# Performance work log

Measured on AMD Instinct MI355X. Metric: run time of the kernel, lower is better.

## Reference

```python
import jax, jax.numpy as jnp
import numpy as np

NQ = 14            # qubits = ceil(log2(16384))
DIM = 2 ** NQ
OUT = 1000         # out_features (slice last OUT probs)


def _apply_ry(state, theta, axis):
    """Apply RY(theta) on the qubit at `axis` of state shaped (B, 2,...,2).
    RY = [[cos(t/2), -sin(t/2)], [sin(t/2), cos(t/2)]] (real)."""
    c = jnp.cos(theta / 2)
    s = jnp.sin(theta / 2)
    x = jnp.moveaxis(state, axis, -1)
    x0, x1 = x[..., 0], x[..., 1]
    y = jnp.stack([c * x0 - s * x1, s * x0 + c * x1], axis=-1)
    return jnp.moveaxis(y, -1, axis)


def _apply_cz(state, axis):
    """CZ on adjacent qubits (axis, axis+1): flip sign of |11> amplitudes."""
    sign = jnp.ones((2, 2), state.dtype).at[1, 1].set(-1.0)
    shape = [1] * state.ndim
    shape[axis] = 2
    shape[axis + 1] = 2
    return state * sign.reshape(shape)


def _circuit(inp, weights, bias):
    B, F = inp.shape
    # AmplitudeEmbedding(pad_with=1, normalize=True)
    if F < DIM:
        inp = jnp.pad(inp, ((0, 0), (0, DIM - F)), constant_values=1.0)
    norm = jnp.sqrt(jnp.sum(inp * inp, axis=1, keepdims=True))
    state = (inp / norm).reshape((B,) + (2,) * NQ)
    # SimplifiedTwoDesign: initial RY layer (bias)
    for w in range(NQ):
        state = _apply_ry(state, bias[w], 1 + w)
    # entangling layers: even CZ/RY block then odd CZ/RY block
    nlayer = weights.shape[0]
    for l in range(nlayer):
        for start in (0, 1):
            for i in range(start, NQ - 1, 2):
                state = _apply_cz(state, 1 + i)
                state = _apply_ry(state, weights[l, i, 0], 1 + i)
                state = _apply_ry(state, weights[l, i, 1], 1 + i + 1)
    amps = state.reshape(B, DIM)
    probs = amps * amps  # real statevector -> |amp|^2
    return probs[:, -OUT:]


def setup_inputs() -> dict:
    key = jax.random.key(0)
    k1, k2, k3 = jax.random.split(key, 3)
    return {
        "input": jax.random.normal(k1, (512, 16384), dtype=jnp.float32),
        "weights": jax.random.normal(k2, (2, NQ - 1, 2), dtype=jnp.float32),
        "bias": jax.random.normal(k3, (NQ,), dtype=jnp.float32),
    }


def reference(input, weights, bias):
    return _circuit(input, weights, bias)
```

## Files before the change

kernel.cpp:

```cpp
#include <hip/hip_runtime.h>

#define NQ 14
#define DIM 16384
#define OUT_N 1000

using v2f = __attribute__((ext_vector_type(2))) float;

__host__ __device__ constexpr int WI(int l, int i, int k) {
    return 14 + (l * 13 + i) * 2 + k;
}

__device__ __forceinline__ int swzM(int e) { return e ^ ((e >> 6) & 31); }
__device__ __forceinline__ int swzB(int a) { return a ^ ((a >> 5) & 31); }

template<int B, int NP>
__device__ __forceinline__ void ry(v2f* x, float c, float s) {
    if constexpr (B == 0) {
#pragma unroll
        for (int p = 0; p < NP; ++p) {
            float a0 = x[p].x, a1 = x[p].y;
            x[p].x = c * a0 - s * a1;
            x[p].y = s * a0 + c * a1;
        }
    } else {
        constexpr int pb = B - 1;
#pragma unroll
        for (int m = 0; m < NP / 2; ++m) {
            int p0 = ((m >> pb) << (pb + 1)) | (m & ((1 << pb) - 1));
            int p1 = p0 | (1 << pb);
            v2f lo = x[p0], hi = x[p1];
            x[p0] = lo * c - hi * s;
            x[p1] = hi * c + lo * s;
        }
    }
}

template<int BH, int BL, int NP>
__device__ __forceinline__ void cz(v2f* x) {
    static_assert(BH > BL, "");
    if constexpr (BL >= 1) {
#pragma unroll
        for (int p = 0; p < NP; ++p)
            if (((p >> (BH - 1)) & 1) && ((p >> (BL - 1)) & 1)) x[p] = -x[p];
    } else {
#pragma unroll
        for (int p = 0; p < NP; ++p)
            if ((p >> (BH - 1)) & 1) x[p].y = -x[p].y;
    }
}

#define BLK(BH, I0, I1, NP)                                       \
    cz<BH, BH - 1, NP>(x);                                        \
    { float2 cc = csl[I0]; ry<BH, NP>(x, cc.x, cc.y); }           \
    { float2 cd = csl[I1]; ry<BH - 1, NP>(x, cd.x, cd.y); }

__global__ __launch_bounds__(256, 2)
void qnn_fused(const float* __restrict__ in, const float* __restrict__ wts,
               const float* __restrict__ bias, float* __restrict__ out) {
    __shared__ float lds[DIM];
    __shared__ float2 csl[66];
    __shared__ float red[4];

    const int t = threadIdx.x;
    const int b = blockIdx.x;

    if (t < 66) {
        float th = (t < NQ) ? bias[t] : wts[t - NQ];
        csl[t] = make_float2(cosf(0.5f * th), sinf(0.5f * th));
    }

    v2f x[32];
    { const float4* __restrict__ src4 = (const float4*)(in + (size_t)b * DIM + t * 64);
#pragma unroll
      for (int i = 0; i < 16; ++i) {
          float4 f = src4[i];
          x[2 * i].x = f.x;     x[2 * i].y = f.y;
          x[2 * i + 1].x = f.z; x[2 * i + 1].y = f.w;
      } }

    float pp = 0.f;
#pragma unroll
    for (int p = 0; p < 32; ++p) pp = fmaf(x[p].x, x[p].x, fmaf(x[p].y, x[p].y, pp));
#pragma unroll
    for (int d = 32; d; d >>= 1) pp += __shfl_xor(pp, d);
    if ((t & 63) == 0) red[t >> 6] = pp;
    __syncthreads();
    const float scale = 1.0f / sqrtf(red[0] + red[1] + red[2] + red[3]);

    { float2 cc;
      cc = csl[8];  ry<5, 32>(x, cc.x, cc.y);
      cc = csl[9];  ry<4, 32>(x, cc.x, cc.y);
      cc = csl[10]; ry<3, 32>(x, cc.x, cc.y);
      cc = csl[11]; ry<2, 32>(x, cc.x, cc.y);
      cc = csl[12]; ry<1, 32>(x, cc.x, cc.y);
      cc = csl[13]; ry<0, 32>(x, cc.x, cc.y); }
    BLK(5, WI(0,8,0),  WI(0,8,1),  32)
    BLK(3, WI(0,10,0), WI(0,10,1), 32)
    BLK(1, WI(0,12,0), WI(0,12,1), 32)
    BLK(4, WI(0,9,0),  WI(0,9,1),  32)
    BLK(2, WI(0,11,0), WI(0,11,1), 32)
    BLK(3, WI(1,10,0), WI(1,10,1), 32)
    BLK(1, WI(1,12,0), WI(1,12,1), 32)
    BLK(2, WI(1,11,0), WI(1,11,1), 32)

#pragma unroll
    for (int r = 0; r < 64; ++r)
        lds[swzM((t << 6) | r)] = (r & 1) ? x[r >> 1].y : x[r >> 1].x;
    __syncthreads();
#pragma unroll
    for (int r = 0; r < 64; ++r) {
        float v = lds[swzM((r << 8) | t)];
        if (r & 1) x[r >> 1].y = v; else x[r >> 1].x = v;
    }

    { float2 cc;
      cc = csl[0]; ry<5, 32>(x, cc.x, cc.y);
      cc = csl[1]; ry<4, 32>(x, cc.x, cc.y);
      cc = csl[2]; ry<3, 32>(x, cc.x, cc.y);
      cc = csl[3]; ry<2, 32>(x, cc.x, cc.y);
      cc = csl[4]; ry<1, 32>(x, cc.x, cc.y);
      cc = csl[5]; ry<0, 32>(x, cc.x, cc.y); }
    BLK(5, WI(0,0,0), WI(0,0,1), 32)
    BLK(3, WI(0,2,0), WI(0,2,1), 32)
    BLK(1, WI(0,4,0), WI(0,4,1), 32)
    BLK(4, WI(0,1,0), WI(0,1,1), 32)
    BLK(2, WI(0,3,0), WI(0,3,1), 32)
    BLK(5, WI(1,0,0), WI(1,0,1), 32)
    BLK(3, WI(1,2,0), WI(1,2,1), 32)
    BLK(4, WI(1,1,0), WI(1,1,1), 32)

    __syncthreads();
#pragma unroll
    for (int p = 28; p < 32; ++p) {
        lds[swzB(((2 * p - 56) << 8) | t)] = x[p].x * scale;
        lds[swzB(((2 * p - 55) << 8) | t)] = x[p].y * scale;
    }
    __syncthreads();

    if (t < 64) {
        const int s = t;
#pragma unroll
        for (int l = 0; l < 32; ++l) {
            float v = lds[swzB((l << 6) | s)];
            if (l & 1) x[l >> 1].y = v; else x[l >> 1].x = v;
        }
        { float2 cc;
          cc = csl[6]; ry<1, 16>(x, cc.x, cc.y);
          cc = csl[7]; ry<0, 16>(x, cc.x, cc.y); }
        BLK(1, WI(0,6,0), WI(0,6,1), 16)
        BLK(2, WI(0,5,0), WI(0,5,1), 16)
        BLK(3, WI(1,4,0), WI(1,4,1), 16)
        BLK(4, WI(1,3,0), WI(1,3,1), 16)
#pragma unroll
        for (int l = 0; l < 32; ++l)
            lds[swzB((l << 6) | s)] = (l & 1) ? x[l >> 1].y : x[l >> 1].x;
    }
    __syncthreads();
    if (t < 64) {
        const int s = t;
#pragma unroll
        for (int l = 0; l < 32; ++l) {
            float v = lds[swzB(((s >> 4) << 9) | (l << 4) | (s & 15))];
            if (l & 1) x[l >> 1].y = v; else x[l >> 1].x = v;
        }
        BLK(2, WI(0,7,0), WI(0,7,1), 16)
        BLK(3, WI(1,6,0), WI(1,6,1), 16)
        BLK(1, WI(1,8,0), WI(1,8,1), 16)
        BLK(4, WI(1,5,0), WI(1,5,1), 16)
        BLK(2, WI(1,7,0), WI(1,7,1), 16)
#pragma unroll
        for (int l = 0; l < 32; ++l)
            lds[swzB(((s >> 4) << 9) | (l << 4) | (s & 15))] =
                (l & 1) ? x[l >> 1].y : x[l >> 1].x;
    }
    __syncthreads();
    if (t < 64) {
        const int s = t;
#pragma unroll
        for (int l = 0; l < 32; ++l) {
            float v = lds[swzB(((s >> 2) << 7) | (l << 2) | (s & 3))];
            if (l & 1) x[l >> 1].y = v; else x[l >> 1].x = v;
        }
        BLK(2, WI(1,9,0), WI(1,9,1), 16)

        if (s >= 32) {
            float* __restrict__ orow = out + (size_t)b * OUT_N;
            const int base = ((s >> 2) << 7) | (s & 3);
#pragma unroll
            for (int l = 0; l < 32; ++l) {
                int j = base + (l << 2) - 1048;
                float v = (l & 1) ? x[l >> 1].y : x[l >> 1].x;
                if (j >= 0) orow[j] = v * v;
            }
        }
    }
}

extern "C" void kernel_launch(void* const* d_in, const int* in_sizes, int n_in,
                              void* d_out, int out_size, void* d_ws, size_t ws_size,
                              hipStream_t stream) {
    const float* in   = (const float*)d_in[0];
    const float* wts  = (const float*)d_in[1];
    const float* bias = (const float*)d_in[2];
    float* out = (float*)d_out;

    const int nb = in_sizes[0] / DIM;
    qnn_fused<<<nb, 256, 0, stream>>>(in, wts, bias, out);
}
```

Measured before the change: 96.89 us.

## Prune circuit to output light cone and drop full-state LDS transpose

Loads the input transposed so each thread holds the high-qubit axis in registers. It applies the high-qubit gates there, then keeps only the last 2048 amplitudes, which cover the sliced output, in a smaller LDS buffer. Low-qubit gates are applied only on that pruned subspace through several LDS reshuffles, so the full 16K-element LDS transpose and the related gate work disappear. The gate order is rearranged to respect the light cone. The cost is uncoalesced strided global loads and more sequential 64-thread phases.

```diff
diff --git a/kernel.cpp b/kernel.cpp
--- a/kernel.cpp
+++ b/kernel.cpp
@@ -3,6 +3,7 @@
 #define NQ 14
 #define DIM 16384
 #define OUT_N 1000
+#define PRUNED 2048
 
 using v2f = __attribute__((ext_vector_type(2))) float;
 
@@ -10,7 +11,6 @@
     return 14 + (l * 13 + i) * 2 + k;
 }
 
-__device__ __forceinline__ int swzM(int e) { return e ^ ((e >> 6) & 31); }
 __device__ __forceinline__ int swzB(int a) { return a ^ ((a >> 5) & 31); }
 
 template<int B, int NP>
@@ -55,9 +55,9 @@
     { float2 cd = csl[I1]; ry<BH - 1, NP>(x, cd.x, cd.y); }
 
 __global__ __launch_bounds__(256, 2)
-void qnn_fused(const float* __restrict__ in, const float* __restrict__ wts,
-               const float* __restrict__ bias, float* __restrict__ out) {
-    __shared__ float lds[DIM];
+void qnn_fused2(const float* __restrict__ in, const float* __restrict__ wts,
+                const float* __restrict__ bias, float* __restrict__ out) {
+    __shared__ float lds[PRUNED];
     __shared__ float2 csl[66];
     __shared__ float red[4];
 
@@ -69,14 +69,13 @@
         csl[t] = make_float2(cosf(0.5f * th), sinf(0.5f * th));
     }
 
+    const float* __restrict__ xin = in + (size_t)b * DIM;
     v2f x[32];
-    { const float4* __restrict__ src4 = (const float4*)(in + (size_t)b * DIM + t * 64);
-#pragma unroll
-      for (int i = 0; i < 16; ++i) {
-          float4 f = src4[i];
-          x[2 * i].x = f.x;     x[2 * i].y = f.y;
-          x[2 * i + 1].x = f.z; x[2 * i + 1].y = f.w;
-      } }
+#pragma unroll
+    for (int p = 0; p < 32; ++p) {
+        x[p].x = xin[((2 * p) << 8) | t];
+        x[p].y = xin[((2 * p + 1) << 8) | t];
+    }
 
     float pp = 0.f;
 #pragma unroll
@@ -86,32 +85,6 @@
     if ((t & 63) == 0) red[t >> 6] = pp;
     __syncthreads();
     const float scale = 1.0f / sqrtf(red[0] + red[1] + red[2] + red[3]);
-
-    { float2 cc;
-      cc = csl[8];  ry<5, 32>(x, cc.x, cc.y);
-      cc = csl[9];  ry<4, 32>(x, cc.x, cc.y);
-      cc = csl[10]; ry<3, 32>(x, cc.x, cc.y);
-      cc = csl[11]; ry<2, 32>(x, cc.x, cc.y);
-      cc = csl[12]; ry<1, 32>(x, cc.x, cc.y);
-      cc = csl[13]; ry<0, 32>(x, cc.x, cc.y); }
-    BLK(5, WI(0,8,0),  WI(0,8,1),  32)
-    BLK(3, WI(0,10,0), WI(0,10,1), 32)
-    BLK(1, WI(0,12,0), WI(0,12,1), 32)
-    BLK(4, WI(0,9,0),  WI(0,9,1),  32)
-    BLK(2, WI(0,11,0), WI(0,11,1), 32)
-    BLK(3, WI(1,10,0), WI(1,10,1), 32)
-    BLK(1, WI(1,12,0), WI(1,12,1), 32)
-    BLK(2, WI(1,11,0), WI(1,11,1), 32)
-
-#pragma unroll
-    for (int r = 0; r < 64; ++r)
-        lds[swzM((t << 6) | r)] = (r & 1) ? x[r >> 1].y : x[r >> 1].x;
-    __syncthreads();
-#pragma unroll
-    for (int r = 0; r < 64; ++r) {
-        float v = lds[swzM((r << 8) | t)];
-        if (r & 1) x[r >> 1].y = v; else x[r >> 1].x = v;
-    }
 
     { float2 cc;
       cc = csl[0]; ry<5, 32>(x, cc.x, cc.y);
@@ -129,7 +102,6 @@
     BLK(3, WI(1,2,0), WI(1,2,1), 32)
     BLK(4, WI(1,1,0), WI(1,1,1), 32)
 
-    __syncthreads();
 #pragma unroll
     for (int p = 28; p < 32; ++p) {
         lds[swzB(((2 * p - 56) << 8) | t)] = x[p].x * scale;
@@ -141,16 +113,74 @@
         const int s = t;
 #pragma unroll
         for (int l = 0; l < 32; ++l) {
+            float v = lds[swzB((s << 5) | l)];
+            if (l & 1) x[l >> 1].y = v; else x[l >> 1].x = v;
+        }
+        { float2 cc;
+          cc = csl[9];  ry<4, 16>(x, cc.x, cc.y);
+          cc = csl[10]; ry<3, 16>(x, cc.x, cc.y);
+          cc = csl[11]; ry<2, 16>(x, cc.x, cc.y);
+          cc = csl[12]; ry<1, 16>(x, cc.x, cc.y);
+          cc = csl[13]; ry<0, 16>(x, cc.x, cc.y); }
+        BLK(3, WI(0,10,0), WI(0,10,1), 16)
+        BLK(1, WI(0,12,0), WI(0,12,1), 16)
+        BLK(2, WI(0,11,0), WI(0,11,1), 16)
+        BLK(1, WI(1,12,0), WI(1,12,1), 16)
+#pragma unroll
+        for (int l = 0; l < 32; ++l)
+            lds[swzB((s << 5) | l)] = (l & 1) ? x[l >> 1].y : x[l >> 1].x;
+    }
+    __syncthreads();
+    if (t < 64) {
+        const int s = t;
+#pragma unroll
+        for (int l = 0; l < 32; ++l) {
+            float v = lds[swzB(((s >> 4) << 9) | (l << 4) | (s & 15))];
+            if (l & 1) x[l >> 1].y = v; else x[l >> 1].x = v;
+        }
+        { float2 cc;
+          cc = csl[6]; ry<3, 16>(x, cc.x, cc.y);
+          cc = csl[7]; ry<2, 16>(x, cc.x, cc.y);
+          cc = csl[8]; ry<1, 16>(x, cc.x, cc.y); }
+        BLK(3, WI(0,6,0), WI(0,6,1), 16)
+        BLK(1, WI(0,8,0), WI(0,8,1), 16)
+        BLK(4, WI(0,5,0), WI(0,5,1), 16)
+        BLK(2, WI(0,7,0), WI(0,7,1), 16)
+        BLK(3, WI(1,6,0), WI(1,6,1), 16)
+#pragma unroll
+        for (int l = 0; l < 32; ++l)
+            lds[swzB(((s >> 4) << 9) | (l << 4) | (s & 15))] =
+                (l & 1) ? x[l >> 1].y : x[l >> 1].x;
+    }
+    __syncthreads();
+    if (t < 64) {
+        const int s = t;
+#pragma unroll
+        for (int l = 0; l < 32; ++l) {
+            float v = lds[swzB(((s >> 2) << 7) | (l << 2) | (s & 3))];
+            if (l & 1) x[l >> 1].y = v; else x[l >> 1].x = v;
+        }
+        BLK(2, WI(0,9,0),  WI(0,9,1),  16)
+        BLK(3, WI(1,8,0),  WI(1,8,1),  16)
+        BLK(1, WI(1,10,0), WI(1,10,1), 16)
+        BLK(4, WI(1,7,0),  WI(1,7,1),  16)
+        BLK(2, WI(1,9,0),  WI(1,9,1),  16)
+#pragma unroll
+        for (int l = 0; l < 32; ++l)
+            lds[swzB(((s >> 2) << 7) | (l << 2) | (s & 3))] =
+                (l & 1) ? x[l >> 1].y : x[l >> 1].x;
+    }
+    __syncthreads();
+    if (t < 64) {
+        const int s = t;
+#pragma unroll
+        for (int l = 0; l < 32; ++l) {
             float v = lds[swzB((l << 6) | s)];
             if (l & 1) x[l >> 1].y = v; else x[l >> 1].x = v;
         }
-        { float2 cc;
-          cc = csl[6]; ry<1, 16>(x, cc.x, cc.y);
-          cc = csl[7]; ry<0, 16>(x, cc.x, cc.y); }
-        BLK(1, WI(0,6,0), WI(0,6,1), 16)
-        BLK(2, WI(0,5,0), WI(0,5,1), 16)
         BLK(3, WI(1,4,0), WI(1,4,1), 16)
         BLK(4, WI(1,3,0), WI(1,3,1), 16)
+        BLK(2, WI(1,5,0), WI(1,5,1), 16)
 #pragma unroll
         for (int l = 0; l < 32; ++l)
             lds[swzB((l << 6) | s)] = (l & 1) ? x[l >> 1].y : x[l >> 1].x;
@@ -160,35 +190,17 @@
         const int s = t;
 #pragma unroll
         for (int l = 0; l < 32; ++l) {
-            float v = lds[swzB(((s >> 4) << 9) | (l << 4) | (s & 15))];
-            if (l & 1) x[l >> 1].y = v; else x[l >> 1].x = v;
-        }
-        BLK(2, WI(0,7,0), WI(0,7,1), 16)
-        BLK(3, WI(1,6,0), WI(1,6,1), 16)
-        BLK(1, WI(1,8,0), WI(1,8,1), 16)
-        BLK(4, WI(1,5,0), WI(1,5,1), 16)
-        BLK(2, WI(1,7,0), WI(1,7,1), 16)
-#pragma unroll
-        for (int l = 0; l < 32; ++l)
-            lds[swzB(((s >> 4) << 9) | (l << 4) | (s & 15))] =
-                (l & 1) ? x[l >> 1].y : x[l >> 1].x;
-    }
-    __syncthreads();
-    if (t < 64) {
-        const int s = t;
-#pragma unroll
-        for (int l = 0; l < 32; ++l) {
-            float v = lds[swzB(((s >> 2) << 7) | (l << 2) | (s & 3))];
-            if (l & 1) x[l >> 1].y = v; else x[l >> 1].x = v;
-        }
-        BLK(2, WI(1,9,0), WI(1,9,1), 16)
+            float v = lds[swzB((s << 5) | l)];
+            if (l & 1) x[l >> 1].y = v; else x[l >> 1].x = v;
+        }
+        BLK(2, WI(1,11,0), WI(1,11,1), 16)
 
         if (s >= 32) {
             float* __restrict__ orow = out + (size_t)b * OUT_N;
-            const int base = ((s >> 2) << 7) | (s & 3);
+            const int base = s * 32 - 1048;
 #pragma unroll
             for (int l = 0; l < 32; ++l) {
-                int j = base + (l << 2) - 1048;
+                int j = base + l;
                 float v = (l & 1) ? x[l >> 1].y : x[l >> 1].x;
                 if (j >= 0) orow[j] = v * v;
             }
@@ -205,5 +217,5 @@
     float* out = (float*)d_out;
 
     const int nb = in_sizes[0] / DIM;
-    qnn_fused<<<nb, 256, 0, stream>>>(in, wts, bias, out);
-}
+    qnn_fused2<<<nb, 256, 0, stream>>>(in, wts, bias, out);
+}
```

Measured after the change: 90.65 us. 1.07x faster.
